# Optimization experiments

Measured on AMD Instinct MI355X. Metric: run time of the kernel, lower is better.

Reference implementation:

```python
import jax, jax.numpy as jnp
import numpy as np

EMB = 300      # LEN_EMB_VECTOR
FH, FO = 200, 200
GH, GO = 200, 200
HH, HO = 200, 3

def _mlp2(x, w1, b1, w2, b2):
    # relu(Linear) -> relu(Linear), torch Linear: y = x @ W.T + b
    h = jax.nn.relu(x @ w1.T + b1)
    return jax.nn.relu(h @ w2.T + b2)

def setup_inputs() -> dict:
    key = jax.random.key(0)
    ks = jax.random.split(key, 16)
    L1, L2 = 8192, 8192
    def lin(k, out_d, in_d):
        kw, kb = jax.random.split(k)
        s = 1.0 / np.sqrt(in_d)
        w = jax.random.uniform(kw, (out_d, in_d), jnp.float32, -s, s)
        b = jax.random.uniform(kb, (out_d,), jnp.float32, -s, s)
        return w, b
    F_w1, F_b1 = lin(ks[0], FH, EMB)
    F_w2, F_b2 = lin(ks[1], FO, FH)
    G_w1, G_b1 = lin(ks[2], GH, 2 * EMB)
    G_w2, G_b2 = lin(ks[3], GO, GH)
    H_w1, H_b1 = lin(ks[4], HH, 2 * GO)
    H_w2, H_b2 = lin(ks[5], HO, HH)
    sen1 = jax.random.normal(ks[6], (L1, EMB), jnp.float32)
    sen2 = jax.random.normal(ks[7], (L2, EMB), jnp.float32)
    return {"sen1": sen1, "sen2": sen2,
            "F_w1": F_w1, "F_b1": F_b1, "F_w2": F_w2, "F_b2": F_b2,
            "G_w1": G_w1, "G_b1": G_b1, "G_w2": G_w2, "G_b2": G_b2,
            "H_w1": H_w1, "H_b1": H_b1, "H_w2": H_w2, "H_b2": H_b2}

def reference(sen1, sen2, F_w1, F_b1, F_w2, F_b2,
              G_w1, G_b1, G_w2, G_b2, H_w1, H_b1, H_w2, H_b2):
    # F projection of every token in both sentences
    Fa = _mlp2(sen1, F_w1, F_b1, F_w2, F_b2)   # [L1, 200]
    Fb = _mlp2(sen2, F_w1, F_b1, F_w2, F_b2)   # [L2, 200]
    # E matrix of dot products: e_ij = Fa_i . Fb_j
    E = jnp.einsum('id,jd->ij', Fa, Fb)        # [L1, L2]
    # beta_i = softmax over j of E[i, :] applied to sen2
    beta = jax.nn.softmax(E, axis=1) @ sen2    # [L1, EMB]
    # alpha_j = softmax over i of E[:, j] applied to sen1
    alpha = jax.nn.softmax(E, axis=0).T @ sen1 # [L2, EMB]
    # G comparison
    v1 = _mlp2(jnp.concatenate([sen1, beta], axis=-1), G_w1, G_b1, G_w2, G_b2)   # [L1, 200]
    v2 = _mlp2(jnp.concatenate([sen2, alpha], axis=-1), G_w1, G_b1, G_w2, G_b2)  # [L2, 200]
    # aggregate: elementwise sums over tokens, then H classifier with softmax
    hx = jnp.concatenate([v1.sum(axis=0), v2.sum(axis=0)])  # [400]
    logits = jax.nn.relu(hx @ H_w1.T + H_b1) @ H_w2.T + H_b2  # [3]
    return jax.nn.softmax(logits)
```

## Files before the change

kernel.cpp:

```cpp
#include <hip/hip_runtime.h>

typedef __attribute__((ext_vector_type(8))) short short8;
typedef __attribute__((ext_vector_type(4))) float f32x4;

__device__ inline ushort f2bf(float f) {
    union { float f; unsigned u; } v{f};
    unsigned r = v.u + 0x7FFF + ((v.u >> 16) & 1);
    return (ushort)(r >> 16);
}

__device__ inline void gload_lds16(const void* g, void* l) {
    __builtin_amdgcn_global_load_lds(
        (const __attribute__((address_space(1))) unsigned int*)(uintptr_t)g,
        (__attribute__((address_space(3))) unsigned int*)(uintptr_t)l,
        16, 0, 0);
}

__global__ __launch_bounds__(256) void convert_inputs_kernel(
    const float* __restrict__ sen1, const float* __restrict__ sen2,
    ushort* __restrict__ Senb, ushort* __restrict__ Xcat)
{
    const int row = blockIdx.x * 8 + (threadIdx.x >> 5);
    const int c0 = threadIdx.x & 31;
    const float* src = (row < 8192) ? (sen1 + (size_t)row * 300)
                                    : (sen2 + (size_t)(row - 8192) * 300);
    ushort* sb = Senb + (size_t)row * 320;
    ushort* xc = Xcat + (size_t)row * 608;
    for (int c = c0; c < 320; c += 32) {
        ushort v = (c < 300) ? f2bf(src[c]) : (ushort)0;
        sb[c] = v;
        if (c < 300) xc[c] = v;
    }
    if (c0 < 8) xc[600 + c0] = 0;
}

__global__ __launch_bounds__(256) void convert_weights_kernel(
    const float* __restrict__ W0, const float* __restrict__ b0,
    const float* __restrict__ W1, const float* __restrict__ b1,
    const float* __restrict__ W2, const float* __restrict__ b2,
    const float* __restrict__ W3, const float* __restrict__ b3,
    ushort* __restrict__ Wb0, float* __restrict__ bp0,
    ushort* __restrict__ Wb1, float* __restrict__ bp1,
    ushort* __restrict__ Wb2, float* __restrict__ bp2,
    ushort* __restrict__ Wb3, float* __restrict__ bp3)
{
    const int id = blockIdx.x;
    const int mat = id / 224, n = id % 224;
    const float* W; const float* b; ushort* Wb; float* bp; int N, K, KP;
    if (mat == 0)      { W = W0; b = b0; Wb = Wb0; bp = bp0; N = 200; K = 300; KP = 320; }
    else if (mat == 1) { W = W1; b = b1; Wb = Wb1; bp = bp1; N = 200; K = 200; KP = 224; }
    else if (mat == 2) { W = W2; b = b2; Wb = Wb2; bp = bp2; N = 200; K = 600; KP = 608; }
    else               { W = W3; b = b3; Wb = Wb3; bp = bp3; N = 200; K = 200; KP = 224; }
    for (int k = threadIdx.x; k < KP; k += 256)
        Wb[(size_t)n * KP + k] = (n < N && k < K) ? f2bf(W[(size_t)n * K + k]) : (ushort)0;
    if (threadIdx.x == 0) bp[n] = (n < N) ? b[n] : 0.f;
}

__global__ __launch_bounds__(256) void transpose_bf16_kernel(
    const float* __restrict__ s1, const float* __restrict__ s2,
    ushort* __restrict__ St1, ushort* __restrict__ St2)
{
    const float* X = blockIdx.z ? s2 : s1;
    ushort* Xt = blockIdx.z ? St2 : St1;
    __shared__ float t[64][65];
    const int r0 = blockIdx.x * 64, c0 = blockIdx.y * 64;
    const int tc = threadIdx.x & 63, tr = threadIdx.x >> 6;
    for (int rr = tr; rr < 64; rr += 4) {
        int c = c0 + tc;
        t[rr][tc] = (c < 300) ? X[(size_t)(r0 + rr) * 300 + c] : 0.f;
    }
    __syncthreads();
    for (int rr = tr; rr < 64; rr += 4) {
        int oc = c0 + rr;
        if (oc < 320)
            Xt[(size_t)oc * 8192 + r0 + tc] = f2bf(t[tc][rr]);
    }
}

__global__ __launch_bounds__(64) void mlp2_kernel(
    const ushort* __restrict__ X, int KP1,
    const ushort* __restrict__ W1, const float* __restrict__ b1,
    const ushort* __restrict__ W2, const float* __restrict__ b2,
    ushort* __restrict__ Ybf, float* __restrict__ Yf)
{
    const int r0 = blockIdx.x * 16;
    const int lane = threadIdx.x;
    const int lr = lane & 15, lg = lane >> 4;

    __shared__ __align__(16) ushort Y1[16][232];

    f32x4 a1[14];
#pragma unroll
    for (int t = 0; t < 14; ++t) a1[t] = f32x4{0.f, 0.f, 0.f, 0.f};

    const ushort* Xrow = X + (size_t)(r0 + lr) * KP1 + lg * 8;
    const ushort* W1r  = W1 + (size_t)lr * KP1 + lg * 8;
    for (int k0 = 0; k0 < KP1; k0 += 32) {
        short8 a = *(const short8*)(Xrow + k0);
#pragma unroll
        for (int t = 0; t < 14; ++t) {
            short8 bfr = *(const short8*)(W1r + (size_t)t * 16 * KP1 + k0);
            a1[t] = __builtin_amdgcn_mfma_f32_16x16x32_bf16(a, bfr, a1[t], 0, 0, 0);
        }
    }
#pragma unroll
    for (int t = 0; t < 14; ++t) {
        int col = t * 16 + lr;
        float bv = b1[col];
#pragma unroll
        for (int rr = 0; rr < 4; ++rr)
            Y1[lg * 4 + rr][col] = f2bf(fmaxf(a1[t][rr] + bv, 0.f));
    }
    __syncthreads();

    f32x4 a2[14];
#pragma unroll
    for (int t = 0; t < 14; ++t) a2[t] = f32x4{0.f, 0.f, 0.f, 0.f};
    const ushort* W2r = W2 + (size_t)lr * 224 + lg * 8;
    for (int k0 = 0; k0 < 224; k0 += 32) {
        short8 a = *(const short8*)&Y1[lr][lg * 8 + k0];
#pragma unroll
        for (int t = 0; t < 14; ++t) {
            short8 bfr = *(const short8*)(W2r + (size_t)t * 16 * 224 + k0);
            a2[t] = __builtin_amdgcn_mfma_f32_16x16x32_bf16(a, bfr, a2[t], 0, 0, 0);
        }
    }
#pragma unroll
    for (int t = 0; t < 14; ++t) {
        int col = t * 16 + lr;
        float bv = b2[col];
#pragma unroll
        for (int rr = 0; rr < 4; ++rr) {
            int row = r0 + lg * 4 + rr;
            float v = fmaxf(a2[t][rr] + bv, 0.f);
            if (Ybf) Ybf[(size_t)row * 224 + col] = f2bf(v);
            else if (col < 200) Yf[(size_t)row * 200 + col] = v;
        }
    }
}

__global__ __launch_bounds__(512, 2) void attend_mfma_kernel(
    const ushort* __restrict__ FaFb, const ushort* __restrict__ St1,
    const ushort* __restrict__ St2, float* __restrict__ Pacc,
    float* __restrict__ Dpart)
{
    const int b = blockIdx.x;
    const int it  = b & 63;
    const int jh  = (b >> 6) & 1;
    const int dir = b >> 7;
    const ushort* A  = FaFb + (dir ? (size_t)8192 * 224 : 0);
    const ushort* B  = FaFb + (dir ? 0 : (size_t)8192 * 224);
    const ushort* St = dir ? St1 : St2;
    const int ib = it * 128;
    const int jo = jh * 4096;

    const int tid = threadIdx.x;
    const int w = tid >> 6;
    const int wi = w >> 1, wj = w & 1;
    const int dq = w & 3,  ih = w >> 2;
    const int lane = tid & 63;
    const int lr = lane & 15, lg = lane >> 4;

    __shared__ __align__(16) ushort Bl[2][28 * 512];
    __shared__ __align__(16) ushort Sl[2][40 * 512];
    __shared__ __align__(16) ushort Pl[128][76];
    __shared__ float dled[8][32];

    f32x4 acc[4][5];
#pragma unroll
    for (int s = 0; s < 4; ++s)
#pragma unroll
        for (int t = 0; t < 5; ++t) acc[s][t] = f32x4{0.f, 0.f, 0.f, 0.f};
    float dsum[2][4] = {{0.f, 0.f, 0.f, 0.f}, {0.f, 0.f, 0.f, 0.f}};

    short8 afr[2][7];
#pragma unroll
    for (int si = 0; si < 2; ++si) {
        const ushort* Ar = A + (size_t)(ib + wi * 32 + si * 16 + lr) * 224 + lg * 8;
#pragma unroll
        for (int k = 0; k < 7; ++k) afr[si][k] = *(const short8*)(Ar + k * 32);
    }

    const int nB = (w < 4) ? 4 : 3;
    const int pB = (w < 4) ? (w * 4) : (16 + (w - 4) * 3);
    int boff[4];
#pragma unroll
    for (int q = 0; q < 4; ++q) {
        int p = pB + q;
        boff[q] = ((p / 7) * 16 + lr) * 448 + ((p % 7) * 32 + lg * 8) * 2;
    }
    const char* Bb = (const char*)B + (size_t)jo * 448;

    int soff[5];
#pragma unroll
    for (int q = 0; q < 5; ++q) {
        int p = w * 5 + q;
        int srow = p * 8 + (lane >> 3);
        int sl = (lane & 7) ^ (srow & 7);
        soff[q] = srow * 16384 + sl * 16;
    }
    const char* Sb = (const char*)St + (size_t)jo * 2;

    int prow[5], prow7[5];
#pragma unroll
    for (int t = 0; t < 5; ++t) {
        prow[t] = (dq * 80 + t * 16 + lr) * 128;
        prow7[t] = (dq * 80 + t * 16 + lr) & 7;
    }

#pragma unroll
    for (int q = 0; q < 4; ++q)
        if (q < nB) gload_lds16(Bb + boff[q], &Bl[0][(pB + q) * 512]);
#pragma unroll
    for (int q = 0; q < 5; ++q)
        gload_lds16(Sb + soff[q], &Sl[0][(w * 5 + q) * 512]);
    __syncthreads();

    int buf = 0;
    for (int jb = 0; jb < 4096; jb += 64, buf ^= 1) {
        f32x4 e[2][2];
#pragma unroll
        for (int si = 0; si < 2; ++si)
#pragma unroll
            for (int jt = 0; jt < 2; ++jt) e[si][jt] = f32x4{0.f, 0.f, 0.f, 0.f};
#pragma unroll
        for (int kk = 0; kk < 7; ++kk) {
            short8 b0 = *(const short8*)&Bl[buf][((2 * wj + 0) * 7 + kk) * 512 + lane * 8];
            short8 b1 = *(const short8*)&Bl[buf][((2 * wj + 1) * 7 + kk) * 512 + lane * 8];
            e[0][0] = __builtin_amdgcn_mfma_f32_16x16x32_bf16(afr[0][kk], b0, e[0][0], 0, 0, 0);
            e[0][1] = __builtin_amdgcn_mfma_f32_16x16x32_bf16(afr[0][kk], b1, e[0][1], 0, 0, 0);
            e[1][0] = __builtin_amdgcn_mfma_f32_16x16x32_bf16(afr[1][kk], b0, e[1][0], 0, 0, 0);
            e[1][1] = __builtin_amdgcn_mfma_f32_16x16x32_bf16(afr[1][kk], b1, e[1][1], 0, 0, 0);
        }

#pragma unroll
        for (int si = 0; si < 2; ++si)
#pragma unroll
            for (int jt = 0; jt < 2; ++jt)
#pragma unroll
                for (int r = 0; r < 4; ++r) {
                    float x = __expf(e[si][jt][r]);
                    dsum[si][r] += x;
                    Pl[wi * 32 + si * 16 + lg * 4 + r][wj * 32 + jt * 16 + lr] = f2bf(x);
                }
        __syncthreads();

        if (jb + 64 < 4096) {
            const char* Bn = Bb + (size_t)(jb + 64) * 448;
            const char* Sn = Sb + (size_t)(jb + 64) * 2;
#pragma unroll
            for (int q = 0; q < 4; ++q)
                if (q < nB) gload_lds16(Bn + boff[q], &Bl[buf ^ 1][(pB + q) * 512]);
#pragma unroll
            for (int q = 0; q < 5; ++q)
                gload_lds16(Sn + soff[q], &Sl[buf ^ 1][(w * 5 + q) * 512]);
        }

#pragma unroll
        for (int h = 0; h < 2; ++h) {
            short8 pf[4];
#pragma unroll
            for (int s = 0; s < 4; ++s)
                pf[s] = *(const short8*)&Pl[ih * 64 + s * 16 + lr][h * 32 + lg * 8];
            short8 st[5];
#pragma unroll
            for (int t = 0; t < 5; ++t) {
                int sl = ((h << 2) | lg) ^ prow7[t];
                st[t] = *(const short8*)((const char*)Sl[buf] + prow[t] + (sl << 4));
            }
#pragma unroll
            for (int s = 0; s < 4; ++s)
#pragma unroll
                for (int t = 0; t < 5; ++t)
                    acc[s][t] = __builtin_amdgcn_mfma_f32_16x16x32_bf16(pf[s], st[t], acc[s][t], 0, 0, 0);
        }
        __syncthreads();
    }

#pragma unroll
    for (int m = 1; m < 16; m <<= 1)
#pragma unroll
        for (int si = 0; si < 2; ++si)
#pragma unroll
            for (int r = 0; r < 4; ++r)
                dsum[si][r] += __shfl_xor(dsum[si][r], m);
    if (lr == 0) {
#pragma unroll
        for (int si = 0; si < 2; ++si)
#pragma unroll
            for (int r = 0; r < 4; ++r)
                dled[w][si * 16 + lg * 4 + r] = dsum[si][r];
    }
    __syncthreads();

    if (tid < 128) {
        int wi2 = tid >> 5, idx = tid & 31;
        Dpart[(size_t)jh * 16384 + dir * 8192 + ib + tid] =
            dled[wi2 * 2][idx] + dled[wi2 * 2 + 1][idx];
    }

    float* Pb = Pacc + ((size_t)jh * 16384 + dir * 8192 + ib + ih * 64) * 320;
#pragma unroll
    for (int t = 0; t < 5; ++t) {
        int d = dq * 80 + t * 16 + lr;
#pragma unroll
        for (int s = 0; s < 4; ++s)
#pragma unroll
            for (int r = 0; r < 4; ++r)
                Pb[(size_t)(s * 16 + lg * 4 + r) * 320 + d] = acc[s][t][r];
    }
}

__global__ __launch_bounds__(256) void combine_kernel(
    const float* __restrict__ Pacc, const float* __restrict__ Dpart,
    ushort* __restrict__ Xcat)
{
    const int row = blockIdx.x * 8 + (threadIdx.x >> 5);
    const int c0 = threadIdx.x & 31;
    const float inv = 1.f / (Dpart[row] + Dpart[16384 + row]);
    const float* pa = Pacc + (size_t)row * 320;
    const float* pb = Pacc + (size_t)(16384 + row) * 320;
    ushort* xc = Xcat + (size_t)row * 608 + 300;
    for (int d = c0; d < 300; d += 32)
        xc[d] = f2bf((pa[d] + pb[d]) * inv);
}

__global__ __launch_bounds__(256) void colsum_kernel(
    const float* __restrict__ v, float* __restrict__ hsum)
{
    const int c = blockIdx.x;
    const float* V = v + (c < 200 ? 0 : (size_t)8192 * 200);
    const int col = c % 200;
    float s = 0.f;
    for (int r = threadIdx.x; r < 8192; r += 256)
        s += V[(size_t)r * 200 + col];
    __shared__ float red[256];
    red[threadIdx.x] = s;
    __syncthreads();
    for (int off = 128; off > 0; off >>= 1) {
        if (threadIdx.x < off) red[threadIdx.x] += red[threadIdx.x + off];
        __syncthreads();
    }
    if (threadIdx.x == 0) hsum[c] = red[0];
}

__global__ __launch_bounds__(256) void head_kernel(
    const float* __restrict__ hsum,
    const float* __restrict__ Hw1, const float* __restrict__ Hb1,
    const float* __restrict__ Hw2, const float* __restrict__ Hb2,
    float* __restrict__ out)
{
    __shared__ float hx[400];
    __shared__ float hr[200];
    __shared__ float lg[3];
    const int t = threadIdx.x;
    for (int i = t; i < 400; i += 256) hx[i] = hsum[i];
    __syncthreads();
    if (t < 200) {
        float a = Hb1[t];
        for (int k = 0; k < 400; ++k) a = fmaf(hx[k], Hw1[t * 400 + k], a);
        hr[t] = fmaxf(a, 0.f);
    }
    __syncthreads();
    if (t < 3) {
        float a = Hb2[t];
        for (int k = 0; k < 200; ++k) a = fmaf(hr[k], Hw2[t * 200 + k], a);
        lg[t] = a;
    }
    __syncthreads();
    if (t == 0) {
        float m = fmaxf(lg[0], fmaxf(lg[1], lg[2]));
        float e0 = __expf(lg[0] - m);
        float e1 = __expf(lg[1] - m);
        float e2 = __expf(lg[2] - m);
        float s = e0 + e1 + e2;
        out[0] = e0 / s;
        out[1] = e1 / s;
        out[2] = e2 / s;
    }
}

extern "C" void kernel_launch(void* const* d_in, const int* in_sizes, int n_in,
                              void* d_out, int out_size, void* d_ws, size_t ws_size,
                              hipStream_t stream)
{
    const float* sen1 = (const float*)d_in[0];
    const float* sen2 = (const float*)d_in[1];
    const float* F_w1 = (const float*)d_in[2];
    const float* F_b1 = (const float*)d_in[3];
    const float* F_w2 = (const float*)d_in[4];
    const float* F_b2 = (const float*)d_in[5];
    const float* G_w1 = (const float*)d_in[6];
    const float* G_b1 = (const float*)d_in[7];
    const float* G_w2 = (const float*)d_in[8];
    const float* G_b2 = (const float*)d_in[9];
    const float* H_w1 = (const float*)d_in[10];
    const float* H_b1 = (const float*)d_in[11];
    const float* H_w2 = (const float*)d_in[12];
    const float* H_b2 = (const float*)d_in[13];
    float* out = (float*)d_out;

    const int L = 8192;
    char* p = (char*)d_ws;
    ushort* St1  = (ushort*)p; p += (size_t)320 * L * 2;
    ushort* St2  = (ushort*)p; p += (size_t)320 * L * 2;
    ushort* FaFb = (ushort*)p; p += (size_t)2 * L * 224 * 2;
    ushort* Xcat = (ushort*)p; p += (size_t)2 * L * 608 * 2;
    ushort* WbF1 = (ushort*)p; p += (size_t)224 * 320 * 2;
    ushort* WbF2 = (ushort*)p; p += (size_t)224 * 224 * 2;
    ushort* WbG1 = (ushort*)p; p += (size_t)224 * 608 * 2;
    ushort* WbG2 = (ushort*)p; p += (size_t)224 * 224 * 2;
    float*  bpF1 = (float*)p;  p += 224 * 4;
    float*  bpF2 = (float*)p;  p += 224 * 4;
    float*  bpG1 = (float*)p;  p += 224 * 4;
    float*  bpG2 = (float*)p;  p += 224 * 4;
    float*  hsum = (float*)p;  p += 400 * 4;
    ushort* Senb  = (ushort*)p;
    float*  Pacc  = (float*)p;
    float*  Dpart = (float*)(p + (size_t)2 * 16384 * 320 * 4);
    float*  v     = (float*)p;

    dim3 blk256(256);

    hipLaunchKernelGGL(convert_inputs_kernel, dim3(2 * L / 8), blk256, 0, stream,
                       sen1, sen2, Senb, Xcat);
    hipLaunchKernelGGL(transpose_bf16_kernel, dim3(L / 64, 5, 2), blk256, 0, stream,
                       sen1, sen2, St1, St2);
    hipLaunchKernelGGL(convert_weights_kernel, dim3(4 * 224), blk256, 0, stream,
                       F_w1, F_b1, F_w2, F_b2, G_w1, G_b1, G_w2, G_b2,
                       WbF1, bpF1, WbF2, bpF2, WbG1, bpG1, WbG2, bpG2);

    hipLaunchKernelGGL(mlp2_kernel, dim3(2 * L / 16), dim3(64), 0, stream,
                       Senb, 320, WbF1, bpF1, WbF2, bpF2, FaFb, (float*)nullptr);

    hipLaunchKernelGGL(attend_mfma_kernel, dim3(256), dim3(512), 0, stream,
                       FaFb, St1, St2, Pacc, Dpart);
    hipLaunchKernelGGL(combine_kernel, dim3(16384 / 8), blk256, 0, stream,
                       Pacc, Dpart, Xcat);

    hipLaunchKernelGGL(mlp2_kernel, dim3(2 * L / 16), dim3(64), 0, stream,
                       Xcat, 608, WbG1, bpG1, WbG2, bpG2, (ushort*)nullptr, v);

    hipLaunchKernelGGL(colsum_kernel, dim3(400), blk256, 0, stream, v, hsum);
    hipLaunchKernelGGL(head_kernel, dim3(1), blk256, 0, stream,
                       hsum, H_w1, H_b1, H_w2, H_b2, out);
}
```

Measured before the change: 303.9 us.

## Fuse input conversion with transpose and softmax-combine into G MLP kernel

Merges the input bf16 conversion into the transpose kernel, removing one launch and one pass over the inputs. The combine step (normalising Pacc by Dpart) is folded into a new gmlp2 kernel that reads the fp32 partials directly, so the Xcat intermediate is dropped. The attend kernel swaps MFMA operand order so P can be stored as packed 8-byte writes, adds s_setprio around the MFMA blocks, and simplifies the row-sum reduction. The G output is now stored as bf16, which halves colsum traffic at some cost in precision.

```diff
diff --git a/kernel.cpp b/kernel.cpp
--- a/kernel.cpp
+++ b/kernel.cpp
@@ -7,6 +7,11 @@
     union { float f; unsigned u; } v{f};
     unsigned r = v.u + 0x7FFF + ((v.u >> 16) & 1);
     return (ushort)(r >> 16);
+}
+__device__ inline float bf2f(ushort u) {
+    union { unsigned u; float f; } v;
+    v.u = ((unsigned)u) << 16;
+    return v.f;
 }
 
 __device__ inline void gload_lds16(const void* g, void* l) {
@@ -16,22 +21,28 @@
         16, 0, 0);
 }
 
-__global__ __launch_bounds__(256) void convert_inputs_kernel(
-    const float* __restrict__ sen1, const float* __restrict__ sen2,
-    ushort* __restrict__ Senb, ushort* __restrict__ Xcat)
-{
-    const int row = blockIdx.x * 8 + (threadIdx.x >> 5);
-    const int c0 = threadIdx.x & 31;
-    const float* src = (row < 8192) ? (sen1 + (size_t)row * 300)
-                                    : (sen2 + (size_t)(row - 8192) * 300);
-    ushort* sb = Senb + (size_t)row * 320;
-    ushort* xc = Xcat + (size_t)row * 608;
-    for (int c = c0; c < 320; c += 32) {
-        ushort v = (c < 300) ? f2bf(src[c]) : (ushort)0;
-        sb[c] = v;
-        if (c < 300) xc[c] = v;
-    }
-    if (c0 < 8) xc[600 + c0] = 0;
+__global__ __launch_bounds__(256) void convert_sen_kernel(
+    const float* __restrict__ s1, const float* __restrict__ s2,
+    ushort* __restrict__ Senb, ushort* __restrict__ St1, ushort* __restrict__ St2)
+{
+    const float* X = blockIdx.z ? s2 : s1;
+    ushort* Xt = blockIdx.z ? St2 : St1;
+    ushort* Sb = Senb + (size_t)blockIdx.z * 8192 * 320;
+    __shared__ float t[64][65];
+    const int r0 = blockIdx.x * 64, c0 = blockIdx.y * 64;
+    const int tc = threadIdx.x & 63, tr = threadIdx.x >> 6;
+    for (int rr = tr; rr < 64; rr += 4) {
+        int c = c0 + tc;
+        float v = (c < 300) ? X[(size_t)(r0 + rr) * 300 + c] : 0.f;
+        t[rr][tc] = v;
+        if (c < 320) Sb[(size_t)(r0 + rr) * 320 + c] = f2bf(v);
+    }
+    __syncthreads();
+    for (int rr = tr; rr < 64; rr += 4) {
+        int oc = c0 + rr;
+        if (oc < 320)
+            Xt[(size_t)oc * 8192 + r0 + tc] = f2bf(t[tc][rr]);
+    }
 }
 
 __global__ __launch_bounds__(256) void convert_weights_kernel(
@@ -46,42 +57,32 @@
 {
     const int id = blockIdx.x;
     const int mat = id / 224, n = id % 224;
+    if (mat == 2) {
+        for (int k = threadIdx.x; k < 640; k += 256) {
+            float v = 0.f;
+            if (n < 200) {
+                if (k < 320) { if (k < 300) v = W2[(size_t)n * 600 + k]; }
+                else { int cc = k - 320; if (cc < 300) v = W2[(size_t)n * 600 + 300 + cc]; }
+            }
+            Wb2[(size_t)n * 640 + k] = f2bf(v);
+        }
+        if (threadIdx.x == 0) bp2[n] = (n < 200) ? b2[n] : 0.f;
+        return;
+    }
     const float* W; const float* b; ushort* Wb; float* bp; int N, K, KP;
     if (mat == 0)      { W = W0; b = b0; Wb = Wb0; bp = bp0; N = 200; K = 300; KP = 320; }
     else if (mat == 1) { W = W1; b = b1; Wb = Wb1; bp = bp1; N = 200; K = 200; KP = 224; }
-    else if (mat == 2) { W = W2; b = b2; Wb = Wb2; bp = bp2; N = 200; K = 600; KP = 608; }
     else               { W = W3; b = b3; Wb = Wb3; bp = bp3; N = 200; K = 200; KP = 224; }
     for (int k = threadIdx.x; k < KP; k += 256)
         Wb[(size_t)n * KP + k] = (n < N && k < K) ? f2bf(W[(size_t)n * K + k]) : (ushort)0;
     if (threadIdx.x == 0) bp[n] = (n < N) ? b[n] : 0.f;
 }
 
-__global__ __launch_bounds__(256) void transpose_bf16_kernel(
-    const float* __restrict__ s1, const float* __restrict__ s2,
-    ushort* __restrict__ St1, ushort* __restrict__ St2)
-{
-    const float* X = blockIdx.z ? s2 : s1;
-    ushort* Xt = blockIdx.z ? St2 : St1;
-    __shared__ float t[64][65];
-    const int r0 = blockIdx.x * 64, c0 = blockIdx.y * 64;
-    const int tc = threadIdx.x & 63, tr = threadIdx.x >> 6;
-    for (int rr = tr; rr < 64; rr += 4) {
-        int c = c0 + tc;
-        t[rr][tc] = (c < 300) ? X[(size_t)(r0 + rr) * 300 + c] : 0.f;
-    }
-    __syncthreads();
-    for (int rr = tr; rr < 64; rr += 4) {
-        int oc = c0 + rr;
-        if (oc < 320)
-            Xt[(size_t)oc * 8192 + r0 + tc] = f2bf(t[tc][rr]);
-    }
-}
-
 __global__ __launch_bounds__(64) void mlp2_kernel(
     const ushort* __restrict__ X, int KP1,
     const ushort* __restrict__ W1, const float* __restrict__ b1,
     const ushort* __restrict__ W2, const float* __restrict__ b2,
-    ushort* __restrict__ Ybf, float* __restrict__ Yf)
+    ushort* __restrict__ Ybf)
 {
     const int r0 = blockIdx.x * 16;
     const int lane = threadIdx.x;
@@ -132,9 +133,92 @@
 #pragma unroll
         for (int rr = 0; rr < 4; ++rr) {
             int row = r0 + lg * 4 + rr;
-            float v = fmaxf(a2[t][rr] + bv, 0.f);
-            if (Ybf) Ybf[(size_t)row * 224 + col] = f2bf(v);
-            else if (col < 200) Yf[(size_t)row * 200 + col] = v;
+            Ybf[(size_t)row * 224 + col] = f2bf(fmaxf(a2[t][rr] + bv, 0.f));
+        }
+    }
+}
+
+__global__ __launch_bounds__(64) void gmlp2_kernel(
+    const ushort* __restrict__ Senb,
+    const float* __restrict__ Pacc, const float* __restrict__ Dpart,
+    const ushort* __restrict__ W1, const float* __restrict__ b1,
+    const ushort* __restrict__ W2, const float* __restrict__ b2,
+    ushort* __restrict__ v)
+{
+    const int r0 = blockIdx.x * 16;
+    const int lane = threadIdx.x;
+    const int lr = lane & 15, lg = lane >> 4;
+    const int row = r0 + lr;
+
+    __shared__ __align__(16) ushort Y1[16][232];
+
+    const float inv = 1.f / (Dpart[row] + Dpart[16384 + row]);
+    const float* pa = Pacc + (size_t)row * 320;
+    const float* pb = pa + (size_t)16384 * 320;
+
+    f32x4 a1[14];
+#pragma unroll
+    for (int t = 0; t < 14; ++t) a1[t] = f32x4{0.f, 0.f, 0.f, 0.f};
+
+    const ushort* Xrow = Senb + (size_t)row * 320 + lg * 8;
+    const ushort* W1r  = W1 + (size_t)lr * 640 + lg * 8;
+    for (int k0 = 0; k0 < 640; k0 += 32) {
+        short8 a;
+        if (k0 < 320) {
+            a = *(const short8*)(Xrow + k0);
+        } else {
+            int kk = k0 - 320 + lg * 8;
+            float4 x0 = *(const float4*)(pa + kk);
+            float4 x1 = *(const float4*)(pa + kk + 4);
+            float4 y0 = *(const float4*)(pb + kk);
+            float4 y1 = *(const float4*)(pb + kk + 4);
+            a[0] = (short)f2bf((x0.x + y0.x) * inv);
+            a[1] = (short)f2bf((x0.y + y0.y) * inv);
+            a[2] = (short)f2bf((x0.z + y0.z) * inv);
+            a[3] = (short)f2bf((x0.w + y0.w) * inv);
+            a[4] = (short)f2bf((x1.x + y1.x) * inv);
+            a[5] = (short)f2bf((x1.y + y1.y) * inv);
+            a[6] = (short)f2bf((x1.z + y1.z) * inv);
+            a[7] = (short)f2bf((x1.w + y1.w) * inv);
+        }
+#pragma unroll
+        for (int t = 0; t < 14; ++t) {
+            short8 bfr = *(const short8*)(W1r + (size_t)t * 16 * 640 + k0);
+            a1[t] = __builtin_amdgcn_mfma_f32_16x16x32_bf16(a, bfr, a1[t], 0, 0, 0);
+        }
+    }
+#pragma unroll
+    for (int t = 0; t < 14; ++t) {
+        int col = t * 16 + lr;
+        float bv = b1[col];
+#pragma unroll
+        for (int rr = 0; rr < 4; ++rr)
+            Y1[lg * 4 + rr][col] = f2bf(fmaxf(a1[t][rr] + bv, 0.f));
+    }
+    __syncthreads();
+
+    f32x4 a2[14];
+#pragma unroll
+    for (int t = 0; t < 14; ++t) a2[t] = f32x4{0.f, 0.f, 0.f, 0.f};
+    const ushort* W2r = W2 + (size_t)lr * 224 + lg * 8;
+    for (int k0 = 0; k0 < 224; k0 += 32) {
+        short8 a = *(const short8*)&Y1[lr][lg * 8 + k0];
+#pragma unroll
+        for (int t = 0; t < 14; ++t) {
+            short8 bfr = *(const short8*)(W2r + (size_t)t * 16 * 224 + k0);
+            a2[t] = __builtin_amdgcn_mfma_f32_16x16x32_bf16(a, bfr, a2[t], 0, 0, 0);
+        }
+    }
+#pragma unroll
+    for (int t = 0; t < 14; ++t) {
+        int col = t * 16 + lr;
+        if (col < 200) {
+            float bv = b2[col];
+#pragma unroll
+            for (int rr = 0; rr < 4; ++rr) {
+                int orow = r0 + lg * 4 + rr;
+                v[(size_t)orow * 200 + col] = f2bf(fmaxf(a2[t][rr] + bv, 0.f));
+            }
         }
     }
 }
@@ -171,7 +255,7 @@
     for (int s = 0; s < 4; ++s)
 #pragma unroll
         for (int t = 0; t < 5; ++t) acc[s][t] = f32x4{0.f, 0.f, 0.f, 0.f};
-    float dsum[2][4] = {{0.f, 0.f, 0.f, 0.f}, {0.f, 0.f, 0.f, 0.f}};
+    float dsum[2] = {0.f, 0.f};
 
     short8 afr[2][7];
 #pragma unroll
@@ -223,26 +307,33 @@
         for (int si = 0; si < 2; ++si)
 #pragma unroll
             for (int jt = 0; jt < 2; ++jt) e[si][jt] = f32x4{0.f, 0.f, 0.f, 0.f};
+        __builtin_amdgcn_s_setprio(1);
 #pragma unroll
         for (int kk = 0; kk < 7; ++kk) {
             short8 b0 = *(const short8*)&Bl[buf][((2 * wj + 0) * 7 + kk) * 512 + lane * 8];
             short8 b1 = *(const short8*)&Bl[buf][((2 * wj + 1) * 7 + kk) * 512 + lane * 8];
-            e[0][0] = __builtin_amdgcn_mfma_f32_16x16x32_bf16(afr[0][kk], b0, e[0][0], 0, 0, 0);
-            e[0][1] = __builtin_amdgcn_mfma_f32_16x16x32_bf16(afr[0][kk], b1, e[0][1], 0, 0, 0);
-            e[1][0] = __builtin_amdgcn_mfma_f32_16x16x32_bf16(afr[1][kk], b0, e[1][0], 0, 0, 0);
-            e[1][1] = __builtin_amdgcn_mfma_f32_16x16x32_bf16(afr[1][kk], b1, e[1][1], 0, 0, 0);
-        }
-
-#pragma unroll
-        for (int si = 0; si < 2; ++si)
-#pragma unroll
-            for (int jt = 0; jt < 2; ++jt)
-#pragma unroll
-                for (int r = 0; r < 4; ++r) {
-                    float x = __expf(e[si][jt][r]);
-                    dsum[si][r] += x;
-                    Pl[wi * 32 + si * 16 + lg * 4 + r][wj * 32 + jt * 16 + lr] = f2bf(x);
-                }
+            e[0][0] = __builtin_amdgcn_mfma_f32_16x16x32_bf16(b0, afr[0][kk], e[0][0], 0, 0, 0);
+            e[1][0] = __builtin_amdgcn_mfma_f32_16x16x32_bf16(b0, afr[1][kk], e[1][0], 0, 0, 0);
+            e[0][1] = __builtin_amdgcn_mfma_f32_16x16x32_bf16(b1, afr[0][kk], e[0][1], 0, 0, 0);
+            e[1][1] = __builtin_amdgcn_mfma_f32_16x16x32_bf16(b1, afr[1][kk], e[1][1], 0, 0, 0);
+        }
+        __builtin_amdgcn_s_setprio(0);
+
+#pragma unroll
+        for (int si = 0; si < 2; ++si) {
+#pragma unroll
+            for (int jt = 0; jt < 2; ++jt) {
+                float x0 = __expf(e[si][jt][0]);
+                float x1 = __expf(e[si][jt][1]);
+                float x2 = __expf(e[si][jt][2]);
+                float x3 = __expf(e[si][jt][3]);
+                dsum[si] += (x0 + x1) + (x2 + x3);
+                uint2 pk;
+                pk.x = (unsigned)f2bf(x0) | ((unsigned)f2bf(x1) << 16);
+                pk.y = (unsigned)f2bf(x2) | ((unsigned)f2bf(x3) << 16);
+                *(uint2*)&Pl[wi * 32 + si * 16 + lr][wj * 32 + jt * 16 + lg * 4] = pk;
+            }
+        }
         __syncthreads();
 
         if (jb + 64 < 4096) {
@@ -268,28 +359,26 @@
                 int sl = ((h << 2) | lg) ^ prow7[t];
                 st[t] = *(const short8*)((const char*)Sl[buf] + prow[t] + (sl << 4));
             }
+            __builtin_amdgcn_s_setprio(1);
 #pragma unroll
             for (int s = 0; s < 4; ++s)
 #pragma unroll
                 for (int t = 0; t < 5; ++t)
                     acc[s][t] = __builtin_amdgcn_mfma_f32_16x16x32_bf16(pf[s], st[t], acc[s][t], 0, 0, 0);
+            __builtin_amdgcn_s_setprio(0);
         }
         __syncthreads();
     }
 
 #pragma unroll
-    for (int m = 1; m < 16; m <<= 1)
+    for (int si = 0; si < 2; ++si) {
+        dsum[si] += __shfl_xor(dsum[si], 16);
+        dsum[si] += __shfl_xor(dsum[si], 32);
+    }
+    if (lg == 0) {
 #pragma unroll
         for (int si = 0; si < 2; ++si)
-#pragma unroll
-            for (int r = 0; r < 4; ++r)
-                dsum[si][r] += __shfl_xor(dsum[si][r], m);
-    if (lr == 0) {
-#pragma unroll
-        for (int si = 0; si < 2; ++si)
-#pragma unroll
-            for (int r = 0; r < 4; ++r)
-                dled[w][si * 16 + lg * 4 + r] = dsum[si][r];
+            dled[w][si * 16 + lr] = dsum[si];
     }
     __syncthreads();
 
@@ -311,29 +400,15 @@
     }
 }
 
-__global__ __launch_bounds__(256) void combine_kernel(
-    const float* __restrict__ Pacc, const float* __restrict__ Dpart,
-    ushort* __restrict__ Xcat)
-{
-    const int row = blockIdx.x * 8 + (threadIdx.x >> 5);
-    const int c0 = threadIdx.x & 31;
-    const float inv = 1.f / (Dpart[row] + Dpart[16384 + row]);
-    const float* pa = Pacc + (size_t)row * 320;
-    const float* pb = Pacc + (size_t)(16384 + row) * 320;
-    ushort* xc = Xcat + (size_t)row * 608 + 300;
-    for (int d = c0; d < 300; d += 32)
-        xc[d] = f2bf((pa[d] + pb[d]) * inv);
-}
-
 __global__ __launch_bounds__(256) void colsum_kernel(
-    const float* __restrict__ v, float* __restrict__ hsum)
+    const ushort* __restrict__ v, float* __restrict__ hsum)
 {
     const int c = blockIdx.x;
-    const float* V = v + (c < 200 ? 0 : (size_t)8192 * 200);
+    const ushort* V = v + (c < 200 ? 0 : (size_t)8192 * 200);
     const int col = c % 200;
     float s = 0.f;
     for (int r = threadIdx.x; r < 8192; r += 256)
-        s += V[(size_t)r * 200 + col];
+        s += bf2f(V[(size_t)r * 200 + col]);
     __shared__ float red[256];
     red[threadIdx.x] = s;
     __syncthreads();
@@ -404,44 +479,39 @@
     char* p = (char*)d_ws;
     ushort* St1  = (ushort*)p; p += (size_t)320 * L * 2;
     ushort* St2  = (ushort*)p; p += (size_t)320 * L * 2;
+    ushort* Senb = (ushort*)p; p += (size_t)2 * L * 320 * 2;
     ushort* FaFb = (ushort*)p; p += (size_t)2 * L * 224 * 2;
-    ushort* Xcat = (ushort*)p; p += (size_t)2 * L * 608 * 2;
+    ushort* vbuf = (ushort*)p; p += (size_t)2 * L * 200 * 2;
     ushort* WbF1 = (ushort*)p; p += (size_t)224 * 320 * 2;
     ushort* WbF2 = (ushort*)p; p += (size_t)224 * 224 * 2;
-    ushort* WbG1 = (ushort*)p; p += (size_t)224 * 608 * 2;
+    ushort* WbG1 = (ushort*)p; p += (size_t)224 * 640 * 2;
     ushort* WbG2 = (ushort*)p; p += (size_t)224 * 224 * 2;
     float*  bpF1 = (float*)p;  p += 224 * 4;
     float*  bpF2 = (float*)p;  p += 224 * 4;
     float*  bpG1 = (float*)p;  p += 224 * 4;
     float*  bpG2 = (float*)p;  p += 224 * 4;
     float*  hsum = (float*)p;  p += 400 * 4;
-    ushort* Senb  = (ushort*)p;
-    float*  Pacc  = (float*)p;
-    float*  Dpart = (float*)(p + (size_t)2 * 16384 * 320 * 4);
-    float*  v     = (float*)p;
+    float*  Pacc = (float*)p;  p += (size_t)2 * 16384 * 320 * 4;
+    float*  Dpart= (float*)p;  p += (size_t)2 * 16384 * 4;
 
     dim3 blk256(256);
 
-    hipLaunchKernelGGL(convert_inputs_kernel, dim3(2 * L / 8), blk256, 0, stream,
-                       sen1, sen2, Senb, Xcat);
-    hipLaunchKernelGGL(transpose_bf16_kernel, dim3(L / 64, 5, 2), blk256, 0, stream,
-                       sen1, sen2, St1, St2);
+    hipLaunchKernelGGL(convert_sen_kernel, dim3(L / 64, 5, 2), blk256, 0, stream,
+                       sen1, sen2, Senb, St1, St2);
     hipLaunchKernelGGL(convert_weights_kernel, dim3(4 * 224), blk256, 0, stream,
                        F_w1, F_b1, F_w2, F_b2, G_w1, G_b1, G_w2, G_b2,
                        WbF1, bpF1, WbF2, bpF2, WbG1, bpG1, WbG2, bpG2);
 
     hipLaunchKernelGGL(mlp2_kernel, dim3(2 * L / 16), dim3(64), 0, stream,
-                       Senb, 320, WbF1, bpF1, WbF2, bpF2, FaFb, (float*)nullptr);
+                       Senb, 320, WbF1, bpF1, WbF2, bpF2, FaFb);
 
     hipLaunchKernelGGL(attend_mfma_kernel, dim3(256), dim3(512), 0, stream,
                        FaFb, St1, St2, Pacc, Dpart);
-    hipLaunchKernelGGL(combine_kernel, dim3(16384 / 8), blk256, 0, stream,
-                       Pacc, Dpart, Xcat);
-
-    hipLaunchKernelGGL(mlp2_kernel, dim3(2 * L / 16), dim3(64), 0, stream,
-                       Xcat, 608, WbG1, bpG1, WbG2, bpG2, (ushort*)nullptr, v);
-
-    hipLaunchKernelGGL(colsum_kernel, dim3(400), blk256, 0, stream, v, hsum);
+
+    hipLaunchKernelGGL(gmlp2_kernel, dim3(2 * L / 16), dim3(64), 0, stream,
+                       Senb, Pacc, Dpart, WbG1, bpG1, WbG2, bpG2, vbuf);
+
+    hipLaunchKernelGGL(colsum_kernel, dim3(400), blk256, 0, stream, vbuf, hsum);
     hipLaunchKernelGGL(head_kernel, dim3(1), blk256, 0, stream,
                        hsum, H_w1, H_b1, H_w2, H_b2, out);
 }
```

Measured after the change: 295.1 us. 2.9% less time.
